# Performance work log

Hardware: AMD Instinct MI355X
Metric: run time of the kernel (lower is better)

## Reference

```python
import jax, jax.numpy as jnp
import numpy as np

B, S_SRC, S_TRG = 128, 512, 128
VIN, VOUT = 128, 128
E, H = 128, 256          # embed, encoder hidden
HD = 2 * H               # decoder hidden = 512 (concat of bi-dir encoder states)
DENC = 2 * H             # encoder output feature dim = 512


def setup_inputs() -> dict:
    key = jax.random.key(0)
    ks = jax.random.split(key, 20)
    g = lambda k, shape: (jax.random.normal(k, shape, jnp.float32) * 0.05)
    inp = {
        "src": jax.random.randint(ks[0], (B, S_SRC), 0, VIN, jnp.int32),
        "trg": jax.random.randint(ks[1], (B, S_TRG), 0, VOUT, jnp.int32),
        # encoder
        "enc_emb": g(ks[2], (VIN, E)),
        "enc_Wih_f": g(ks[3], (4 * H, E)),
        "enc_Whh_f": g(ks[4], (4 * H, H)),
        "enc_b_f": g(ks[5], (4 * H,)),
        "enc_Wih_b": g(ks[6], (4 * H, E)),
        "enc_Whh_b": g(ks[7], (4 * H, H)),
        "enc_b_b": g(ks[8], (4 * H,)),
        # decoder
        "dec_emb": g(ks[9], (VOUT, E)),
        "dec_Wih": g(ks[10], (4 * HD, E + DENC)),
        "dec_Whh": g(ks[11], (4 * HD, HD)),
        "dec_b": g(ks[12], (4 * HD,)),
        # attention: Linear(dec_hid + enc_dim -> HD), v: Linear(HD -> 1)
        "attn_W": g(ks[13], (HD + DENC, HD)),
        "attn_b": g(ks[14], (HD,)),
        "attn_v": g(ks[15], (HD,)),
        # output projection
        "out_W": g(ks[16], (HD, VOUT)),
        "out_b": g(ks[17], (VOUT,)),
    }
    return inp


def _lstm_cell(h, c, x, Wih, Whh, b):
    gates = x @ Wih.T + h @ Whh.T + b               # [B, 4H]
    i, f, gg, o = jnp.split(gates, 4, axis=-1)       # PyTorch gate order i,f,g,o
    i, f, o = jax.nn.sigmoid(i), jax.nn.sigmoid(f), jax.nn.sigmoid(o)
    c = f * c + i * jnp.tanh(gg)
    h = o * jnp.tanh(c)
    return h, c


def _lstm_scan(xs, Wih, Whh, b, reverse=False):
    # xs: [S, B, E] -> hs: [S, B, H] (time-aligned), plus final (h, c)
    Bn, Hn = xs.shape[1], Whh.shape[1]
    init = (jnp.zeros((Bn, Hn), xs.dtype), jnp.zeros((Bn, Hn), xs.dtype))
    def step(carry, x):
        h, c = _lstm_cell(carry[0], carry[1], x, Wih, Whh, b)
        return (h, c), h
    (h, c), hs = jax.lax.scan(step, init, xs, reverse=reverse)
    return hs, h, c


def reference(src, trg, enc_emb, enc_Wih_f, enc_Whh_f, enc_b_f,
              enc_Wih_b, enc_Whh_b, enc_b_b, dec_emb, dec_Wih, dec_Whh,
              dec_b, attn_W, attn_b, attn_v, out_W, out_b):
    # ----- encoder (bidirectional LSTM) -----
    emb = enc_emb[src]                                # [B, S, E]
    xs = jnp.swapaxes(emb, 0, 1)                      # [S, B, E]
    hs_f, hf, cf = _lstm_scan(xs, enc_Wih_f, enc_Whh_f, enc_b_f, reverse=False)
    hs_b, hb, cb = _lstm_scan(xs, enc_Wih_b, enc_Whh_b, enc_b_b, reverse=True)
    enc_out = jnp.swapaxes(jnp.concatenate([hs_f, hs_b], -1), 0, 1)  # [B, S, 2H]
    hidden = jnp.concatenate([hf, hb], -1)            # [B, HD]  (hidden.view(1,B,-1))
    cell = jnp.concatenate([cf, cb], -1)              # [B, HD]

    # attention linear split: energy = tanh([h, enc] @ W + b)
    Wh, We = attn_W[:HD], attn_W[HD:]
    enc_proj = jnp.einsum("bsd,de->bse", enc_out, We)  # [B, S, HD] precomputed

    def dec_step(carry, tok):
        h, c = carry
        e = jnp.tanh(h[:, None, :] @ Wh + enc_proj + attn_b)     # [B, S, HD]
        scores = jnp.einsum("bse,e->bs", e, attn_v)              # [B, S]
        aw = jax.nn.softmax(scores, axis=1)
        ctx = jnp.einsum("bs,bsd->bd", aw, enc_out)              # [B, DENC]
        x = jnp.concatenate([dec_emb[tok], ctx], -1)             # [B, E+DENC]
        h, c = _lstm_cell(h, c, x, dec_Wih, dec_Whh, dec_b)
        logits = h @ out_W + out_b                               # [B, VOUT]
        return (h, c), logits

    # teacher forcing (ratio=1.0): input at step t is trg[:, t-1], t = 1..T-1
    toks = jnp.swapaxes(trg[:, :-1], 0, 1)            # [T-1, B]
    _, logits = jax.lax.scan(dec_step, (hidden, cell), toks)
    logits = jnp.swapaxes(logits, 0, 1)               # [B, T-1, VOUT]
    outputs = jnp.concatenate(
        [jnp.zeros((src.shape[0], 1, VOUT), logits.dtype), logits], axis=1)
    return outputs
```

## Files before the change

kernel.cpp:

```cpp
#include <hip/hip_runtime.h>


typedef _Float16 f16;
typedef _Float16 half8 __attribute__((ext_vector_type(8)));
typedef float f32x4 __attribute__((ext_vector_type(4)));
typedef char char8v __attribute__((ext_vector_type(8)));

#define MFMA16(a, b, c) __builtin_amdgcn_mfma_f32_16x16x32_f16((a), (b), (c), 0, 0, 0)

#define PSCALE (2.5f / 127.f)
#define PINV   (127.f / 2.5f)

__device__ __forceinline__ float fsig(float x) {
    return __builtin_amdgcn_rcpf(1.f + __expf(-x));
}
__device__ __forceinline__ float ftanh(float x) {
    return 1.f - 2.f * __builtin_amdgcn_rcpf(1.f + __expf(2.f * x));
}
__device__ __forceinline__ int frag_idx(int m, int k, int KS) {
    return (((m >> 4) * KS + (k >> 5)) * 64 + (((k >> 3) & 3) * 16 + (m & 15))) * 8 + (k & 7);
}

__global__ __launch_bounds__(256) void k_prep(
    const float* __restrict__ attn_W, const float* __restrict__ out_W,
    const float* __restrict__ enc_emb,
    const float* __restrict__ wihf, const float* __restrict__ wihb,
    const float* __restrict__ whhf, const float* __restrict__ whhb,
    const float* __restrict__ dec_emb, const float* __restrict__ dec_wih,
    const float* __restrict__ dec_whh,
    f16* __restrict__ WhT_sw, f16* __restrict__ outWT_sw,
    f16* __restrict__ whhf_sw, f16* __restrict__ whhb_sw,
    f16* __restrict__ decwih_sw, f16* __restrict__ decwhh_sw,
    f16* __restrict__ WeT, f16* __restrict__ emb16,
    f16* __restrict__ wihf16, f16* __restrict__ wihb16,
    f16* __restrict__ decemb16, float* __restrict__ out)
{
    long i = (long)blockIdx.x * 256 + threadIdx.x;
    if (i >= 3784704L) return;
    long idx = i;
    if (idx < 262144) {
        int j = idx & 7, lane = (idx >> 3) & 63, c = lane & 15, q = lane >> 4;
        int ks = (idx >> 9) & 15, nt = idx >> 13;
        WhT_sw[idx] = (f16)attn_W[(ks * 32 + q * 8 + j) * 512 + nt * 16 + c];
        return;
    }
    idx -= 262144;
    if (idx < 65536) {
        int j = idx & 7, lane = (idx >> 3) & 63, c = lane & 15, q = lane >> 4;
        int ks = (idx >> 9) & 15, nt = idx >> 13;
        outWT_sw[idx] = (f16)out_W[(ks * 32 + q * 8 + j) * 128 + nt * 16 + c];
        return;
    }
    idx -= 65536;
    if (idx < 262144) {
        int j = idx & 7, lane = (idx >> 3) & 63, c = lane & 15, q = lane >> 4;
        int ks = (idx >> 9) & 7, nt = idx >> 12;
        whhf_sw[idx] = (f16)whhf[(nt * 16 + c) * 256 + ks * 32 + q * 8 + j];
        return;
    }
    idx -= 262144;
    if (idx < 262144) {
        int j = idx & 7, lane = (idx >> 3) & 63, c = lane & 15, q = lane >> 4;
        int ks = (idx >> 9) & 7, nt = idx >> 12;
        whhb_sw[idx] = (f16)whhb[(nt * 16 + c) * 256 + ks * 32 + q * 8 + j];
        return;
    }
    idx -= 262144;
    if (idx < 1310720) {
        int j = idx & 7, lane = (idx >> 3) & 63, c = lane & 15, q = lane >> 4;
        int r2 = idx >> 9; int ks = r2 % 20, nt = r2 / 20;
        decwih_sw[idx] = (f16)dec_wih[(nt * 16 + c) * 640 + ks * 32 + q * 8 + j];
        return;
    }
    idx -= 1310720;
    if (idx < 1048576) {
        int j = idx & 7, lane = (idx >> 3) & 63, c = lane & 15, q = lane >> 4;
        int ks = (idx >> 9) & 15, nt = idx >> 13;
        decwhh_sw[idx] = (f16)dec_whh[(nt * 16 + c) * 512 + ks * 32 + q * 8 + j];
        return;
    }
    idx -= 1048576;
    if (idx < 262144) { int e = idx >> 9, d = idx & 511; WeT[idx] = (f16)attn_W[(512 + d) * 512 + e]; return; }
    idx -= 262144;
    if (idx < 16384)  { emb16[idx] = (f16)enc_emb[idx]; return; }
    idx -= 16384;
    if (idx < 131072) { wihf16[idx] = (f16)wihf[idx]; return; }
    idx -= 131072;
    if (idx < 131072) { wihb16[idx] = (f16)wihb[idx]; return; }
    idx -= 131072;
    if (idx < 16384)  { decemb16[idx] = (f16)dec_emb[idx]; return; }
    idx -= 16384;
    if (idx < 16384)  { int b = idx >> 7, v = idx & 127; out[b * 16384 + v] = 0.f; return; }
}

__global__ __launch_bounds__(256) void k_vocab(
    const f16* __restrict__ emb, const f16* __restrict__ wihf,
    const f16* __restrict__ wihb, const float* __restrict__ bf_,
    const float* __restrict__ bb_, f16* __restrict__ xg_vocab)
{
    int bn = blockIdx.x;
    int tid = threadIdx.x, wave = tid >> 6, lane = tid & 63;
    int col = lane & 15, quad = lane >> 4;
    int wr = wave >> 1, wc = wave & 1;

    f32x4 acc[4][4] = {};
    for (int ks = 0; ks < 4; ++ks) {
        int k0 = ks * 32 + quad * 8;
        half8 a[4], bfr[4];
        for (int i = 0; i < 4; ++i)
            a[i] = *(const half8*)(emb + (wr * 64 + i * 16 + col) * 128 + k0);
        for (int j = 0; j < 4; ++j) {
            int n = bn * 128 + wc * 64 + j * 16 + col;
            const f16* wp = (n < 1024) ? (wihf + n * 128) : (wihb + (n - 1024) * 128);
            bfr[j] = *(const half8*)(wp + k0);
        }
        for (int i = 0; i < 4; ++i)
            for (int j = 0; j < 4; ++j)
                acc[i][j] = MFMA16(a[i], bfr[j], acc[i][j]);
    }
    for (int j = 0; j < 4; ++j) {
        int n = bn * 128 + wc * 64 + j * 16 + col;
        float bias = (n < 1024) ? bf_[n] : bb_[n - 1024];
        for (int i = 0; i < 4; ++i) {
            int vbase = wr * 64 + i * 16 + quad * 4;
            for (int r = 0; r < 4; ++r)
                xg_vocab[(vbase + r) * 2048 + n] = (f16)(acc[i][j][r] + bias);
        }
    }
}

__global__ __launch_bounds__(512, 1) void k_enc(
    const int* __restrict__ src, const f16* __restrict__ xg_vocab,
    const f16* __restrict__ whhf_sw, const f16* __restrict__ whhb_sw,
    f16* __restrict__ enc_out, f16* __restrict__ hdec0, float* __restrict__ c_ws)
{
    int blk = blockIdx.x;
    int dir = blk >> 3, bbase = (blk & 7) * 16;
    int tid = threadIdx.x, wave = tid >> 6, lane = tid & 63;
    int col = lane & 15, quad = lane >> 4;
    const f16* whh = dir ? whhb_sw : whhf_sw;

    __shared__ f16 hb[16][264];
    __shared__ f16 xvb[16][1032];
    __shared__ int stall[8192];

    for (int z = tid; z < 16 * 264; z += 512) ((f16*)hb)[z] = (f16)0.f;
    for (int z = tid; z < 8192; z += 512) stall[z] = src[bbase * 512 + z];
    float cc[2][4] = {};

    half8 bst[32];
    #pragma unroll
    for (int g = 0; g < 2; ++g)
        #pragma unroll
        for (int nt = 0; nt < 2; ++nt)
            #pragma unroll
            for (int kk = 0; kk < 8; ++kk) {
                int tile = g * 16 + wave * 2 + nt;
                bst[(g * 2 + nt) * 8 + kk] =
                    *(const half8*)(whh + ((tile * 8 + kk) * 64 + lane) * 8);
            }
    __syncthreads();

    int xrow = tid >> 7, xoff = (tid & 127) * 8;
    half8 xr[4];
    {
        int ts0 = dir ? 511 : 0;
        #pragma unroll
        for (int it = 0; it < 4; ++it) {
            int row = it * 4 + xrow;
            int tok = stall[row * 512 + ts0];
            xr[it] = *(const half8*)(xg_vocab + tok * 2048 + dir * 1024 + xoff);
        }
    }

    int ts_prev = 0;
    for (int t = 0; t < 512; ++t) {
        int ts = dir ? (511 - t) : t;

        if (t > 0) {
            int b = tid >> 5, seg = tid & 31;
            *(half8*)(enc_out + ((size_t)(bbase + b) * 512 + ts_prev) * 512 + dir * 256 + seg * 8) =
                *(const half8*)(&hb[b][seg * 8]);
        }
        #pragma unroll
        for (int it = 0; it < 4; ++it)
            *(half8*)(&xvb[it * 4 + xrow][xoff]) = xr[it];
        half8 a[8];
        #pragma unroll
        for (int kk = 0; kk < 8; ++kk)
            a[kk] = *(const half8*)(&hb[col][kk * 32 + quad * 8]);
        __syncthreads();

        if (t < 511) {
            int tsn = dir ? (510 - t) : (t + 1);
            #pragma unroll
            for (int it = 0; it < 4; ++it) {
                int row = it * 4 + xrow;
                int tok = stall[row * 512 + tsn];
                xr[it] = *(const half8*)(xg_vocab + tok * 2048 + dir * 1024 + xoff);
            }
        }

        f32x4 acc[4][2] = {};
        #pragma unroll
        for (int kk = 0; kk < 8; ++kk) {
            half8 bv[4];
            #pragma unroll
            for (int g = 2; g < 4; ++g)
                #pragma unroll
                for (int nt = 0; nt < 2; ++nt) {
                    int tile = g * 16 + wave * 2 + nt;
                    bv[(g - 2) * 2 + nt] =
                        *(const half8*)(whh + ((tile * 8 + kk) * 64 + lane) * 8);
                }
            #pragma unroll
            for (int g = 0; g < 2; ++g)
                #pragma unroll
                for (int nt = 0; nt < 2; ++nt)
                    acc[g][nt] = MFMA16(a[kk], bst[(g * 2 + nt) * 8 + kk], acc[g][nt]);
            #pragma unroll
            for (int g = 2; g < 4; ++g)
                #pragma unroll
                for (int nt = 0; nt < 2; ++nt)
                    acc[g][nt] = MFMA16(a[kk], bv[(g - 2) * 2 + nt], acc[g][nt]);
        }

        #pragma unroll
        for (int nt = 0; nt < 2; ++nt) {
            int hcol = wave * 32 + nt * 16 + col;
            #pragma unroll
            for (int r = 0; r < 4; ++r) {
                int b = quad * 4 + r;
                float gi = (float)xvb[b][0 * 256 + hcol] + acc[0][nt][r];
                float gf = (float)xvb[b][1 * 256 + hcol] + acc[1][nt][r];
                float gg = (float)xvb[b][2 * 256 + hcol] + acc[2][nt][r];
                float go = (float)xvb[b][3 * 256 + hcol] + acc[3][nt][r];
                float ig = fsig(gi), fg = fsig(gf), g2 = ftanh(gg), og = fsig(go);
                float cv = fg * cc[nt][r] + ig * g2;
                cc[nt][r] = cv;
                float h = og * ftanh(cv);
                hb[b][hcol] = (f16)h;
            }
        }
        __syncthreads();
        ts_prev = ts;
    }

    {
        int b = tid >> 5, seg = tid & 31;
        *(half8*)(enc_out + ((size_t)(bbase + b) * 512 + ts_prev) * 512 + dir * 256 + seg * 8) =
            *(const half8*)(&hb[b][seg * 8]);
    }
    #pragma unroll
    for (int nt = 0; nt < 2; ++nt) {
        int hcol = wave * 32 + nt * 16 + col;
        #pragma unroll
        for (int r = 0; r < 4; ++r) {
            int b = quad * 4 + r;
            int m = bbase + b, k = dir * 256 + hcol;
            hdec0[frag_idx(m, k, 16)] = hb[b][hcol];
            c_ws[m * 512 + k] = cc[nt][r];
        }
    }
}

__global__ __launch_bounds__(256) void k_proj(
    const f16* __restrict__ enc_out, const f16* __restrict__ WeT,
    char* __restrict__ proj8)
{
    int blk = blockIdx.x;
    int bm = blk & 511, bn = blk >> 9;
    int tid = threadIdx.x, wave = tid >> 6, lane = tid & 63;
    int col = lane & 15, quad = lane >> 4;
    int wr = wave >> 1, wc = wave & 1;

    f32x4 acc[4][4] = {};
    for (int ks = 0; ks < 16; ++ks) {
        int k0 = ks * 32 + quad * 8;
        half8 a[4], bfr[4];
        for (int i = 0; i < 4; ++i) {
            int m = bm * 128 + wr * 64 + i * 16 + col;
            a[i] = *(const half8*)(enc_out + (size_t)m * 512 + k0);
        }
        for (int j = 0; j < 4; ++j) {
            int n = bn * 128 + wc * 64 + j * 16 + col;
            bfr[j] = *(const half8*)(WeT + n * 512 + k0);
        }
        for (int i = 0; i < 4; ++i)
            for (int j = 0; j < 4; ++j)
                acc[i][j] = MFMA16(a[i], bfr[j], acc[i][j]);
    }
    for (int j = 0; j < 4; ++j) {
        int n = bn * 128 + wc * 64 + j * 16 + col;
        for (int i = 0; i < 4; ++i) {
            int mbase = bm * 128 + wr * 64 + i * 16 + quad * 4;
            for (int r = 0; r < 4; ++r) {
                float v = acc[i][j][r] * PINV;
                int q = (int)rintf(v);
                q = (q > 127) ? 127 : ((q < -127) ? -127 : q);
                proj8[(size_t)(mbase + r) * 512 + n] = (char)q;
            }
        }
    }
}

__global__ __launch_bounds__(256) void k_qinit(
    const f16* __restrict__ h0_sw, const f16* __restrict__ WhT_sw,
    float* __restrict__ qpart)
{
    int j = blockIdx.x;
    int tid = threadIdx.x, wave = tid >> 6, lane = tid & 63;
    int col = lane & 15, quad = lane >> 4;
    half8 a[2];
    #pragma unroll
    for (int i = 0; i < 2; ++i)
        a[i] = *(const half8*)(h0_sw + (((wave * 2 + i) * 16 + j) * 64 + lane) * 8);
    for (int nt = 0; nt < 32; ++nt) {
        half8 bfr = *(const half8*)(WhT_sw + ((nt * 16 + j) * 64 + lane) * 8);
        f32x4 q0 = {}, q1 = {};
        q0 = MFMA16(a[0], bfr, q0);
        q1 = MFMA16(a[1], bfr, q1);
        #pragma unroll
        for (int r = 0; r < 4; ++r) {
            qpart[(j * 128 + wave * 32 + quad * 4 + r) * 512 + nt * 16 + col] = q0[r];
            qpart[(j * 128 + wave * 32 + 16 + quad * 4 + r) * 512 + nt * 16 + col] = q1[r];
        }
    }
}

__global__ __launch_bounds__(512) void k_att(
    const char* __restrict__ proj8, const f16* __restrict__ enc_out,
    const float* __restrict__ qpart, const float* __restrict__ attn_b,
    const float* __restrict__ attn_v, const int* __restrict__ trg,
    const f16* __restrict__ dec_emb, f16* __restrict__ x_sw,
    float* __restrict__ part_m, float* __restrict__ part_l,
    float* __restrict__ part_ctx, int t)
{
    int blk = blockIdx.x;
    int b = blk >> 1, sh = blk & 1;
    int tid = threadIdx.x, wave = tid >> 6, lane = tid & 63;
    __shared__ float q[512];
    __shared__ float sc[256];
    __shared__ float ctxred[8][512];
    __shared__ float wred[8], wred2[8];

    {
        float s = attn_b[tid];
        #pragma unroll
        for (int jj = 0; jj < 16; ++jj) s += qpart[(jj * 128 + b) * 512 + tid];
        q[tid] = s;
    }
    __syncthreads();

    float qreg[8], vreg[8];
    #pragma unroll
    for (int u = 0; u < 8; ++u) {
        int e = lane * 8 + u;
        qreg[u] = q[e];
        vreg[u] = attn_v[e];
    }
    int sbase = sh * 256;
    for (int ib = 0; ib < 4; ++ib) {
        char8v p[8];
        #pragma unroll
        for (int z = 0; z < 8; ++z) {
            int sl = (ib * 8 + z) * 8 + wave;
            p[z] = *(const char8v*)(proj8 + ((size_t)b * 512 + sbase + sl) * 512 + lane * 8);
        }
        #pragma unroll
        for (int z = 0; z < 8; ++z) {
            int sl = (ib * 8 + z) * 8 + wave;
            float part = 0.f;
            #pragma unroll
            for (int u = 0; u < 8; ++u)
                part += vreg[u] * ftanh(fmaf((float)p[z][u], PSCALE, qreg[u]));
            #pragma unroll
            for (int o = 32; o; o >>= 1) part += __shfl_xor(part, o);
            if (lane == 0) sc[sl] = part;
        }
    }
    __syncthreads();

    float s0 = (tid < 256) ? sc[tid] : -__builtin_inff();
    float mv = s0;
    #pragma unroll
    for (int o = 32; o; o >>= 1) mv = fmaxf(mv, __shfl_xor(mv, o));
    if (lane == 0) wred[wave] = mv;
    __syncthreads();
    float M = wred[0];
    #pragma unroll
    for (int w = 1; w < 8; ++w) M = fmaxf(M, wred[w]);
    float e0 = (tid < 256) ? __expf(s0 - M) : 0.f;
    if (tid < 256) sc[tid] = e0;
    float sm = e0;
    #pragma unroll
    for (int o = 32; o; o >>= 1) sm += __shfl_xor(sm, o);
    if (lane == 0) wred2[wave] = sm;
    __syncthreads();
    float lb = wred2[0];
    #pragma unroll
    for (int w = 1; w < 8; ++w) lb += wred2[w];

    float a8[8] = {};
    for (int ib = 0; ib < 4; ++ib) {
        half8 ev[8];
        float wgt[8];
        #pragma unroll
        for (int z = 0; z < 8; ++z) {
            int sl = (ib * 8 + z) * 8 + wave;
            ev[z] = *(const half8*)(enc_out + ((size_t)b * 512 + sbase + sl) * 512 + lane * 8);
            wgt[z] = sc[sl];
        }
        #pragma unroll
        for (int z = 0; z < 8; ++z)
            #pragma unroll
            for (int u = 0; u < 8; ++u) a8[u] += wgt[z] * (float)ev[z][u];
    }
    #pragma unroll
    for (int u = 0; u < 8; ++u) ctxred[wave][lane * 8 + u] = a8[u];
    __syncthreads();
    float cp = 0.f;
    #pragma unroll
    for (int w = 0; w < 8; ++w) cp += ctxred[w][tid];
    part_ctx[(size_t)blk * 512 + tid] = cp;
    if (tid == 0) { part_m[blk] = M; part_l[blk] = lb; }

    if (sh == 0 && tid < 128) {
        int tok = trg[b * 128 + t];
        x_sw[frag_idx(b, tid, 20)] = dec_emb[tok * 128 + tid];
    }
}

__global__ __launch_bounds__(256) void k_gates(
    f16* __restrict__ x_sw, const f16* __restrict__ hprev_sw,
    const f16* __restrict__ wih_sw, const f16* __restrict__ whh_sw,
    const float* __restrict__ dec_b, float* __restrict__ c_ws,
    f16* __restrict__ hnext_sw, f16* __restrict__ hhist_sw,
    const f16* __restrict__ WhT_sw, float* __restrict__ qpart,
    const float* __restrict__ part_m, const float* __restrict__ part_l,
    const float* __restrict__ part_ctx, int t)
{
    int jb = blockIdx.x;
    int j = jb >> 1, mh = jb & 1;
    int tid = threadIdx.x, wave = tid >> 6, lane = tid & 63;
    int col = lane & 15, quad = lane >> 4;
    __shared__ f16 hsl[64][40];
    __shared__ float gm[64][2];

    if (tid < 64) {
        int bb = mh * 64 + tid;
        float m0 = part_m[bb * 2 + 0], m1 = part_m[bb * 2 + 1];
        float l0 = part_l[bb * 2 + 0], l1 = part_l[bb * 2 + 1];
        float M = fmaxf(m0, m1);
        float g0 = __expf(m0 - M), g1 = __expf(m1 - M);
        float inv = 1.f / (g0 * l0 + g1 * l1);
        gm[tid][0] = g0 * inv;
        gm[tid][1] = g1 * inv;
    }
    __syncthreads();
    for (int z = tid; z < 32768; z += 256) {
        int lr = z >> 9, d = z & 511;
        int bb = mh * 64 + lr;
        float c = gm[lr][0] * part_ctx[(size_t)(bb * 2 + 0) * 512 + d]
                + gm[lr][1] * part_ctx[(size_t)(bb * 2 + 1) * 512 + d];
        x_sw[frag_idx(bb, 128 + d, 20)] = (f16)c;
    }
    __syncthreads();

    f32x4 acc[8] = {};
    for (int ks = 0; ks < 36; ++ks) {
        int mtile = mh * 4 + wave;
        half8 a = (ks < 20)
            ? *(const half8*)(x_sw + ((mtile * 20 + ks) * 64 + lane) * 8)
            : *(const half8*)(hprev_sw + ((mtile * 16 + (ks - 20)) * 64 + lane) * 8);
        half8 bv[8];
        #pragma unroll
        for (int jt = 0; jt < 8; ++jt) {
            int g = jt >> 1, u2 = jt & 1;
            int ntile = g * 32 + j * 2 + u2;
            bv[jt] = (ks < 20)
                ? *(const half8*)(wih_sw + ((ntile * 20 + ks) * 64 + lane) * 8)
                : *(const half8*)(whh_sw + ((ntile * 16 + (ks - 20)) * 64 + lane) * 8);
        }
        #pragma unroll
        for (int jt = 0; jt < 8; ++jt)
            acc[jt] = MFMA16(a, bv[jt], acc[jt]);
    }
    float bias[8];
    #pragma unroll
    for (int jt = 0; jt < 8; ++jt) {
        int g = jt >> 1, u2 = jt & 1;
        bias[jt] = dec_b[g * 512 + j * 32 + u2 * 16 + col];
    }
    #pragma unroll
    for (int r = 0; r < 4; ++r) {
        int lb = wave * 16 + quad * 4 + r;
        int bb = mh * 64 + lb;
        #pragma unroll
        for (int u2 = 0; u2 < 2; ++u2) {
            int hl = u2 * 16 + col, hcol = j * 32 + hl;
            float gi = acc[0 + u2][r] + bias[0 + u2];
            float gf = acc[2 + u2][r] + bias[2 + u2];
            float gg = acc[4 + u2][r] + bias[4 + u2];
            float go = acc[6 + u2][r] + bias[6 + u2];
            float ig = fsig(gi), fg = fsig(gf), g2 = ftanh(gg), og = fsig(go);
            float cv = fg * c_ws[bb * 512 + hcol] + ig * g2;
            c_ws[bb * 512 + hcol] = cv;
            float h = og * ftanh(cv);
            f16 h16 = (f16)h;
            int fidx = frag_idx(bb, hcol, 16);
            hnext_sw[fidx] = h16;
            hhist_sw[t * 65536 + fidx] = h16;
            hsl[lb][hl] = h16;
        }
    }
    half8 aq = *(const half8*)(&hsl[wave * 16 + col][quad * 8]);
    for (int nt = 0; nt < 32; ++nt) {
        half8 bq = *(const half8*)(WhT_sw + ((nt * 16 + j) * 64 + lane) * 8);
        f32x4 q0 = {};
        q0 = MFMA16(aq, bq, q0);
        #pragma unroll
        for (int r = 0; r < 4; ++r)
            qpart[(j * 128 + mh * 64 + wave * 16 + quad * 4 + r) * 512 + nt * 16 + col] = q0[r];
    }
}

__global__ __launch_bounds__(256) void k_logits(
    const f16* __restrict__ hhist_sw, const f16* __restrict__ outWT_sw,
    const float* __restrict__ out_b, float* __restrict__ out)
{
    int bt = blockIdx.x;
    int tid = threadIdx.x, wave = tid >> 6, lane = tid & 63;
    int col = lane & 15, quad = lane >> 4;
    f32x4 acc[2][8] = {};
    for (int ks = 0; ks < 16; ++ks) {
        half8 a[2];
        #pragma unroll
        for (int i = 0; i < 2; ++i)
            a[i] = *(const half8*)(hhist_sw + bt * 65536 + (((wave * 2 + i) * 16 + ks) * 64 + lane) * 8);
        half8 bv[8];
        #pragma unroll
        for (int jt = 0; jt < 8; ++jt)
            bv[jt] = *(const half8*)(outWT_sw + ((jt * 16 + ks) * 64 + lane) * 8);
        #pragma unroll
        for (int jt = 0; jt < 8; ++jt) {
            acc[0][jt] = MFMA16(a[0], bv[jt], acc[0][jt]);
            acc[1][jt] = MFMA16(a[1], bv[jt], acc[1][jt]);
        }
    }
    #pragma unroll
    for (int jt = 0; jt < 8; ++jt) {
        float bias = out_b[jt * 16 + col];
        #pragma unroll
        for (int i = 0; i < 2; ++i)
            #pragma unroll
            for (int r = 0; r < 4; ++r) {
                int br = wave * 32 + i * 16 + quad * 4 + r;
                out[br * 16384 + (bt + 1) * 128 + jt * 16 + col] = acc[i][jt][r] + bias;
            }
    }
}

extern "C" void kernel_launch(void* const* d_in, const int* in_sizes, int n_in,
                              void* d_out, int out_size, void* d_ws, size_t ws_size,
                              hipStream_t stream)
{
    (void)in_sizes; (void)n_in; (void)out_size;
    if (ws_size < 130000000) return;

    const int*   src     = (const int*)d_in[0];
    const int*   trg     = (const int*)d_in[1];
    const float* enc_emb = (const float*)d_in[2];
    const float* wihf    = (const float*)d_in[3];
    const float* whhf    = (const float*)d_in[4];
    const float* bf_     = (const float*)d_in[5];
    const float* wihb    = (const float*)d_in[6];
    const float* whhb    = (const float*)d_in[7];
    const float* bb_     = (const float*)d_in[8];
    const float* dec_emb = (const float*)d_in[9];
    const float* dec_wih = (const float*)d_in[10];
    const float* dec_whh = (const float*)d_in[11];
    const float* dec_b   = (const float*)d_in[12];
    const float* attn_W  = (const float*)d_in[13];
    const float* attn_b  = (const float*)d_in[14];
    const float* attn_v  = (const float*)d_in[15];
    const float* out_W   = (const float*)d_in[16];
    const float* out_b   = (const float*)d_in[17];
    float* out = (float*)d_out;

    char* p = (char*)d_ws;
    auto carve = [&](size_t n) { char* r = p; p += ((n + 255) & ~(size_t)255); return r; };
    f16*   enc_out   = (f16*)  carve(67108864);
    char*  proj8     = (char*) carve(33554432);
    f16*   WhT_sw    = (f16*)  carve(524288);
    f16*   WeT       = (f16*)  carve(524288);
    f16*   outWT_sw  = (f16*)  carve(131072);
    f16*   emb16     = (f16*)  carve(32768);
    f16*   wihf16    = (f16*)  carve(262144);
    f16*   wihb16    = (f16*)  carve(262144);
    f16*   whhf_sw   = (f16*)  carve(524288);
    f16*   whhb_sw   = (f16*)  carve(524288);
    f16*   decemb16  = (f16*)  carve(32768);
    f16*   decwih_sw = (f16*)  carve(2621440);
    f16*   decwhh_sw = (f16*)  carve(2097152);
    float* qpart     = (float*)carve(4194304);
    f16*   hdec0     = (f16*)  carve(131072);
    f16*   hdec1     = (f16*)  carve(131072);
    float* c_ws      = (float*)carve(262144);
    f16*   x_sw      = (f16*)  carve(163840);
    f16*   hhist_sw  = (f16*)  carve(16646144);
    f16*   xg_vocab  = (f16*)  carve(524288);
    float* part_m    = (float*)carve(2048);
    float* part_l    = (float*)carve(2048);
    float* part_ctx  = (float*)carve(524288);

    k_prep<<<14784, 256, 0, stream>>>(attn_W, out_W, enc_emb, wihf, wihb, whhf, whhb,
                                      dec_emb, dec_wih, dec_whh,
                                      WhT_sw, outWT_sw, whhf_sw, whhb_sw,
                                      decwih_sw, decwhh_sw, WeT, emb16,
                                      wihf16, wihb16, decemb16, out);
    k_vocab<<<16, 256, 0, stream>>>(emb16, wihf16, wihb16, bf_, bb_, xg_vocab);
    k_enc<<<16, 512, 0, stream>>>(src, xg_vocab, whhf_sw, whhb_sw, enc_out, hdec0, c_ws);
    k_proj<<<2048, 256, 0, stream>>>(enc_out, WeT, proj8);
    k_qinit<<<16, 256, 0, stream>>>(hdec0, WhT_sw, qpart);
    for (int t = 0; t < 127; ++t) {
        k_att<<<256, 512, 0, stream>>>(proj8, enc_out, qpart, attn_b, attn_v,
                                       trg, decemb16, x_sw, part_m, part_l,
                                       part_ctx, t);
        f16* hin  = (t & 1) ? hdec1 : hdec0;
        f16* hout = (t & 1) ? hdec0 : hdec1;
        k_gates<<<32, 256, 0, stream>>>(x_sw, hin, decwih_sw, decwhh_sw, dec_b,
                                        c_ws, hout, hhist_sw, WhT_sw, qpart,
                                        part_m, part_l, part_ctx, t);
    }
    k_logits<<<127, 256, 0, stream>>>(hhist_sw, outWT_sw, out_b, out);
}
```

Baseline: 13.39 ms.

## Fuse decoder timestep loop into one persistent kernel with grid barriers

Replaces the 254 per-step launches of the attention and gate kernels with a single persistent kernel of 256 blocks that loops over all 127 decoder steps. Blocks synchronise through atomic-counter grid barriers in global memory, and the gate work runs on 16 of the blocks, each now covering all 128 batch rows. The aim is to remove kernel launch overhead and inter-kernel gaps on this latency-bound recurrence. In exchange, 240 blocks sit idle during the gate phase, the gate work loses half its previous parallelism, and correctness depends on all 256 blocks being resident at once.

```diff
diff --git a/kernel.cpp b/kernel.cpp
--- a/kernel.cpp
+++ b/kernel.cpp
@@ -19,6 +19,23 @@
 }
 __device__ __forceinline__ int frag_idx(int m, int k, int KS) {
     return (((m >> 4) * KS + (k >> 5)) * 64 + (((k >> 3) & 3) * 16 + (m & 15))) * 8 + (k & 7);
+}
+
+__device__ __forceinline__ void gbar(unsigned* ctr, bool arriver, unsigned target) {
+    __syncthreads();
+    if (threadIdx.x == 0) {
+        if (arriver)
+            __hip_atomic_fetch_add(ctr, 1u, __ATOMIC_RELEASE, __HIP_MEMORY_SCOPE_AGENT);
+        while (__hip_atomic_load(ctr, __ATOMIC_RELAXED, __HIP_MEMORY_SCOPE_AGENT) < target)
+            __builtin_amdgcn_s_sleep(8);
+        (void)__hip_atomic_load(ctr, __ATOMIC_ACQUIRE, __HIP_MEMORY_SCOPE_AGENT);
+    }
+    __syncthreads();
+}
+
+__global__ void k_zero(unsigned* __restrict__ s)
+{
+    if (threadIdx.x < 64) s[threadIdx.x] = 0u;
 }
 
 __global__ __launch_bounds__(256) void k_prep(
@@ -328,200 +345,200 @@
     }
 }
 
-__global__ __launch_bounds__(512) void k_att(
+__global__ __launch_bounds__(512, 2) void k_decode(
     const char* __restrict__ proj8, const f16* __restrict__ enc_out,
-    const float* __restrict__ qpart, const float* __restrict__ attn_b,
-    const float* __restrict__ attn_v, const int* __restrict__ trg,
+    float* __restrict__ qpart, const float* __restrict__ attn_bp,
+    const float* __restrict__ attn_vp, const int* __restrict__ trg,
     const f16* __restrict__ dec_emb, f16* __restrict__ x_sw,
     float* __restrict__ part_m, float* __restrict__ part_l,
-    float* __restrict__ part_ctx, int t)
+    float* __restrict__ part_ctx, f16* __restrict__ hdec0,
+    f16* __restrict__ hdec1, const f16* __restrict__ wih_sw,
+    const f16* __restrict__ whh_sw, const float* __restrict__ dec_bp,
+    float* __restrict__ c_ws, f16* __restrict__ hhist_sw,
+    const f16* __restrict__ WhT_sw, unsigned* __restrict__ syncv)
 {
     int blk = blockIdx.x;
+    int tid = threadIdx.x, wave = tid >> 6, lane = tid & 63;
+    int col = lane & 15, quad = lane >> 4;
     int b = blk >> 1, sh = blk & 1;
-    int tid = threadIdx.x, wave = tid >> 6, lane = tid & 63;
+    int sbase = sh * 256;
+
     __shared__ float q[512];
     __shared__ float sc[256];
     __shared__ float ctxred[8][512];
     __shared__ float wred[8], wred2[8];
-
-    {
-        float s = attn_b[tid];
-        #pragma unroll
-        for (int jj = 0; jj < 16; ++jj) s += qpart[(jj * 128 + b) * 512 + tid];
-        q[tid] = s;
-    }
-    __syncthreads();
-
-    float qreg[8], vreg[8];
+    __shared__ f16 hsl[128][40];
+    __shared__ float gm[128][2];
+
+    float vreg[8];
     #pragma unroll
-    for (int u = 0; u < 8; ++u) {
-        int e = lane * 8 + u;
-        qreg[u] = q[e];
-        vreg[u] = attn_v[e];
-    }
-    int sbase = sh * 256;
-    for (int ib = 0; ib < 4; ++ib) {
-        char8v p[8];
-        #pragma unroll
-        for (int z = 0; z < 8; ++z) {
-            int sl = (ib * 8 + z) * 8 + wave;
-            p[z] = *(const char8v*)(proj8 + ((size_t)b * 512 + sbase + sl) * 512 + lane * 8);
-        }
-        #pragma unroll
-        for (int z = 0; z < 8; ++z) {
-            int sl = (ib * 8 + z) * 8 + wave;
-            float part = 0.f;
-            #pragma unroll
-            for (int u = 0; u < 8; ++u)
-                part += vreg[u] * ftanh(fmaf((float)p[z][u], PSCALE, qreg[u]));
-            #pragma unroll
-            for (int o = 32; o; o >>= 1) part += __shfl_xor(part, o);
-            if (lane == 0) sc[sl] = part;
-        }
-    }
-    __syncthreads();
-
-    float s0 = (tid < 256) ? sc[tid] : -__builtin_inff();
-    float mv = s0;
-    #pragma unroll
-    for (int o = 32; o; o >>= 1) mv = fmaxf(mv, __shfl_xor(mv, o));
-    if (lane == 0) wred[wave] = mv;
-    __syncthreads();
-    float M = wred[0];
-    #pragma unroll
-    for (int w = 1; w < 8; ++w) M = fmaxf(M, wred[w]);
-    float e0 = (tid < 256) ? __expf(s0 - M) : 0.f;
-    if (tid < 256) sc[tid] = e0;
-    float sm = e0;
-    #pragma unroll
-    for (int o = 32; o; o >>= 1) sm += __shfl_xor(sm, o);
-    if (lane == 0) wred2[wave] = sm;
-    __syncthreads();
-    float lb = wred2[0];
-    #pragma unroll
-    for (int w = 1; w < 8; ++w) lb += wred2[w];
-
-    float a8[8] = {};
-    for (int ib = 0; ib < 4; ++ib) {
-        half8 ev[8];
-        float wgt[8];
-        #pragma unroll
-        for (int z = 0; z < 8; ++z) {
-            int sl = (ib * 8 + z) * 8 + wave;
-            ev[z] = *(const half8*)(enc_out + ((size_t)b * 512 + sbase + sl) * 512 + lane * 8);
-            wgt[z] = sc[sl];
-        }
-        #pragma unroll
-        for (int z = 0; z < 8; ++z)
-            #pragma unroll
-            for (int u = 0; u < 8; ++u) a8[u] += wgt[z] * (float)ev[z][u];
-    }
-    #pragma unroll
-    for (int u = 0; u < 8; ++u) ctxred[wave][lane * 8 + u] = a8[u];
-    __syncthreads();
-    float cp = 0.f;
-    #pragma unroll
-    for (int w = 0; w < 8; ++w) cp += ctxred[w][tid];
-    part_ctx[(size_t)blk * 512 + tid] = cp;
-    if (tid == 0) { part_m[blk] = M; part_l[blk] = lb; }
-
-    if (sh == 0 && tid < 128) {
-        int tok = trg[b * 128 + t];
-        x_sw[frag_idx(b, tid, 20)] = dec_emb[tok * 128 + tid];
-    }
-}
-
-__global__ __launch_bounds__(256) void k_gates(
-    f16* __restrict__ x_sw, const f16* __restrict__ hprev_sw,
-    const f16* __restrict__ wih_sw, const f16* __restrict__ whh_sw,
-    const float* __restrict__ dec_b, float* __restrict__ c_ws,
-    f16* __restrict__ hnext_sw, f16* __restrict__ hhist_sw,
-    const f16* __restrict__ WhT_sw, float* __restrict__ qpart,
-    const float* __restrict__ part_m, const float* __restrict__ part_l,
-    const float* __restrict__ part_ctx, int t)
-{
-    int jb = blockIdx.x;
-    int j = jb >> 1, mh = jb & 1;
-    int tid = threadIdx.x, wave = tid >> 6, lane = tid & 63;
-    int col = lane & 15, quad = lane >> 4;
-    __shared__ f16 hsl[64][40];
-    __shared__ float gm[64][2];
-
-    if (tid < 64) {
-        int bb = mh * 64 + tid;
-        float m0 = part_m[bb * 2 + 0], m1 = part_m[bb * 2 + 1];
-        float l0 = part_l[bb * 2 + 0], l1 = part_l[bb * 2 + 1];
-        float M = fmaxf(m0, m1);
-        float g0 = __expf(m0 - M), g1 = __expf(m1 - M);
-        float inv = 1.f / (g0 * l0 + g1 * l1);
-        gm[tid][0] = g0 * inv;
-        gm[tid][1] = g1 * inv;
-    }
-    __syncthreads();
-    for (int z = tid; z < 32768; z += 256) {
-        int lr = z >> 9, d = z & 511;
-        int bb = mh * 64 + lr;
-        float c = gm[lr][0] * part_ctx[(size_t)(bb * 2 + 0) * 512 + d]
-                + gm[lr][1] * part_ctx[(size_t)(bb * 2 + 1) * 512 + d];
-        x_sw[frag_idx(bb, 128 + d, 20)] = (f16)c;
-    }
-    __syncthreads();
-
-    f32x4 acc[8] = {};
-    for (int ks = 0; ks < 36; ++ks) {
-        int mtile = mh * 4 + wave;
-        half8 a = (ks < 20)
-            ? *(const half8*)(x_sw + ((mtile * 20 + ks) * 64 + lane) * 8)
-            : *(const half8*)(hprev_sw + ((mtile * 16 + (ks - 20)) * 64 + lane) * 8);
-        half8 bv[8];
-        #pragma unroll
-        for (int jt = 0; jt < 8; ++jt) {
-            int g = jt >> 1, u2 = jt & 1;
-            int ntile = g * 32 + j * 2 + u2;
-            bv[jt] = (ks < 20)
-                ? *(const half8*)(wih_sw + ((ntile * 20 + ks) * 64 + lane) * 8)
-                : *(const half8*)(whh_sw + ((ntile * 16 + (ks - 20)) * 64 + lane) * 8);
-        }
-        #pragma unroll
-        for (int jt = 0; jt < 8; ++jt)
-            acc[jt] = MFMA16(a, bv[jt], acc[jt]);
-    }
-    float bias[8];
-    #pragma unroll
-    for (int jt = 0; jt < 8; ++jt) {
-        int g = jt >> 1, u2 = jt & 1;
-        bias[jt] = dec_b[g * 512 + j * 32 + u2 * 16 + col];
-    }
-    #pragma unroll
-    for (int r = 0; r < 4; ++r) {
-        int lb = wave * 16 + quad * 4 + r;
-        int bb = mh * 64 + lb;
-        #pragma unroll
-        for (int u2 = 0; u2 < 2; ++u2) {
-            int hl = u2 * 16 + col, hcol = j * 32 + hl;
-            float gi = acc[0 + u2][r] + bias[0 + u2];
-            float gf = acc[2 + u2][r] + bias[2 + u2];
-            float gg = acc[4 + u2][r] + bias[4 + u2];
-            float go = acc[6 + u2][r] + bias[6 + u2];
-            float ig = fsig(gi), fg = fsig(gf), g2 = ftanh(gg), og = fsig(go);
-            float cv = fg * c_ws[bb * 512 + hcol] + ig * g2;
-            c_ws[bb * 512 + hcol] = cv;
-            float h = og * ftanh(cv);
-            f16 h16 = (f16)h;
-            int fidx = frag_idx(bb, hcol, 16);
-            hnext_sw[fidx] = h16;
-            hhist_sw[t * 65536 + fidx] = h16;
-            hsl[lb][hl] = h16;
-        }
-    }
-    half8 aq = *(const half8*)(&hsl[wave * 16 + col][quad * 8]);
-    for (int nt = 0; nt < 32; ++nt) {
-        half8 bq = *(const half8*)(WhT_sw + ((nt * 16 + j) * 64 + lane) * 8);
-        f32x4 q0 = {};
-        q0 = MFMA16(aq, bq, q0);
-        #pragma unroll
-        for (int r = 0; r < 4; ++r)
-            qpart[(j * 128 + mh * 64 + wave * 16 + quad * 4 + r) * 512 + nt * 16 + col] = q0[r];
+    for (int u = 0; u < 8; ++u) vreg[u] = attn_vp[lane * 8 + u];
+    float ab = attn_bp[tid];
+
+    for (int t = 0; t < 127; ++t) {
+        {
+            float s = ab;
+            #pragma unroll
+            for (int jj = 0; jj < 16; ++jj) s += qpart[(jj * 128 + b) * 512 + tid];
+            q[tid] = s;
+        }
+        __syncthreads();
+        float qreg[8];
+        #pragma unroll
+        for (int u = 0; u < 8; ++u) qreg[u] = q[lane * 8 + u];
+
+        for (int ib = 0; ib < 4; ++ib) {
+            char8v p[8];
+            #pragma unroll
+            for (int z = 0; z < 8; ++z) {
+                int sl = (ib * 8 + z) * 8 + wave;
+                p[z] = *(const char8v*)(proj8 + ((size_t)b * 512 + sbase + sl) * 512 + lane * 8);
+            }
+            #pragma unroll
+            for (int z = 0; z < 8; ++z) {
+                int sl = (ib * 8 + z) * 8 + wave;
+                float part = 0.f;
+                #pragma unroll
+                for (int u = 0; u < 8; ++u)
+                    part += vreg[u] * ftanh(fmaf((float)p[z][u], PSCALE, qreg[u]));
+                #pragma unroll
+                for (int o = 32; o; o >>= 1) part += __shfl_xor(part, o);
+                if (lane == 0) sc[sl] = part;
+            }
+        }
+        __syncthreads();
+
+        float s0 = (tid < 256) ? sc[tid] : -__builtin_inff();
+        float mv = s0;
+        #pragma unroll
+        for (int o = 32; o; o >>= 1) mv = fmaxf(mv, __shfl_xor(mv, o));
+        if (lane == 0) wred[wave] = mv;
+        __syncthreads();
+        float M = wred[0];
+        #pragma unroll
+        for (int w = 1; w < 8; ++w) M = fmaxf(M, wred[w]);
+        float e0 = (tid < 256) ? __expf(s0 - M) : 0.f;
+        if (tid < 256) sc[tid] = e0;
+        float sm = e0;
+        #pragma unroll
+        for (int o = 32; o; o >>= 1) sm += __shfl_xor(sm, o);
+        if (lane == 0) wred2[wave] = sm;
+        __syncthreads();
+        float lsum = wred2[0];
+        #pragma unroll
+        for (int w = 1; w < 8; ++w) lsum += wred2[w];
+
+        float a8[8] = {};
+        for (int ib = 0; ib < 4; ++ib) {
+            half8 ev[8];
+            float wgt[8];
+            #pragma unroll
+            for (int z = 0; z < 8; ++z) {
+                int sl = (ib * 8 + z) * 8 + wave;
+                ev[z] = *(const half8*)(enc_out + ((size_t)b * 512 + sbase + sl) * 512 + lane * 8);
+                wgt[z] = sc[sl];
+            }
+            #pragma unroll
+            for (int z = 0; z < 8; ++z)
+                #pragma unroll
+                for (int u = 0; u < 8; ++u) a8[u] += wgt[z] * (float)ev[z][u];
+        }
+        #pragma unroll
+        for (int u = 0; u < 8; ++u) ctxred[wave][lane * 8 + u] = a8[u];
+        __syncthreads();
+        float cp = 0.f;
+        #pragma unroll
+        for (int w = 0; w < 8; ++w) cp += ctxred[w][tid];
+        part_ctx[(size_t)blk * 512 + tid] = cp;
+        if (tid == 0) { part_m[blk] = M; part_l[blk] = lsum; }
+
+        if (sh == 0 && tid < 128) {
+            int tok = trg[b * 128 + t];
+            x_sw[frag_idx(b, tid, 20)] = dec_emb[tok * 128 + tid];
+        }
+
+        gbar(&syncv[0], true, 256u * (unsigned)(t + 1));
+
+        if (blk < 16) {
+            int j = blk;
+            if (tid < 128) {
+                float m0 = part_m[tid * 2 + 0], m1 = part_m[tid * 2 + 1];
+                float l0 = part_l[tid * 2 + 0], l1 = part_l[tid * 2 + 1];
+                float Mx = fmaxf(m0, m1);
+                float g0 = __expf(m0 - Mx), g1 = __expf(m1 - Mx);
+                float inv = 1.f / (g0 * l0 + g1 * l1);
+                gm[tid][0] = g0 * inv;
+                gm[tid][1] = g1 * inv;
+            }
+            __syncthreads();
+            for (int z = tid; z < 65536; z += 512) {
+                int lr = z >> 9, d = z & 511;
+                float cval = gm[lr][0] * part_ctx[(size_t)(lr * 2 + 0) * 512 + d]
+                           + gm[lr][1] * part_ctx[(size_t)(lr * 2 + 1) * 512 + d];
+                x_sw[frag_idx(lr, 128 + d, 20)] = (f16)cval;
+            }
+            __syncthreads();
+
+            const f16* hprev = (t & 1) ? hdec1 : hdec0;
+            f16* hnext = (t & 1) ? hdec0 : hdec1;
+
+            f32x4 acc[8] = {};
+            for (int ks = 0; ks < 36; ++ks) {
+                half8 a = (ks < 20)
+                    ? *(const half8*)(x_sw + ((wave * 20 + ks) * 64 + lane) * 8)
+                    : *(const half8*)(hprev + ((wave * 16 + (ks - 20)) * 64 + lane) * 8);
+                half8 bv[8];
+                #pragma unroll
+                for (int jt = 0; jt < 8; ++jt) {
+                    int g = jt >> 1, u2 = jt & 1;
+                    int ntile = g * 32 + j * 2 + u2;
+                    bv[jt] = (ks < 20)
+                        ? *(const half8*)(wih_sw + ((ntile * 20 + ks) * 64 + lane) * 8)
+                        : *(const half8*)(whh_sw + ((ntile * 16 + (ks - 20)) * 64 + lane) * 8);
+                }
+                #pragma unroll
+                for (int jt = 0; jt < 8; ++jt)
+                    acc[jt] = MFMA16(a, bv[jt], acc[jt]);
+            }
+            float bias[8];
+            #pragma unroll
+            for (int jt = 0; jt < 8; ++jt) {
+                int g = jt >> 1, u2 = jt & 1;
+                bias[jt] = dec_bp[g * 512 + j * 32 + u2 * 16 + col];
+            }
+            #pragma unroll
+            for (int r = 0; r < 4; ++r) {
+                int bb = wave * 16 + quad * 4 + r;
+                #pragma unroll
+                for (int u2 = 0; u2 < 2; ++u2) {
+                    int hl = u2 * 16 + col, hcol = j * 32 + hl;
+                    float gi = acc[0 + u2][r] + bias[0 + u2];
+                    float gf = acc[2 + u2][r] + bias[2 + u2];
+                    float gg = acc[4 + u2][r] + bias[4 + u2];
+                    float go = acc[6 + u2][r] + bias[6 + u2];
+                    float ig = fsig(gi), fg = fsig(gf), g2 = ftanh(gg), og = fsig(go);
+                    float cv = fg * c_ws[bb * 512 + hcol] + ig * g2;
+                    c_ws[bb * 512 + hcol] = cv;
+                    float h = og * ftanh(cv);
+                    f16 h16 = (f16)h;
+                    int fidx = frag_idx(bb, hcol, 16);
+                    hnext[fidx] = h16;
+                    hhist_sw[t * 65536 + fidx] = h16;
+                    hsl[bb][hl] = h16;
+                }
+            }
+            half8 aq = *(const half8*)(&hsl[wave * 16 + col][quad * 8]);
+            for (int nt = 0; nt < 32; ++nt) {
+                half8 bq = *(const half8*)(WhT_sw + ((nt * 16 + j) * 64 + lane) * 8);
+                f32x4 q0 = {};
+                q0 = MFMA16(aq, bq, q0);
+                #pragma unroll
+                for (int r = 0; r < 4; ++r)
+                    qpart[(j * 128 + wave * 16 + quad * 4 + r) * 512 + nt * 16 + col] = q0[r];
+            }
+        }
+
+        gbar(&syncv[1], blk < 16, 16u * (unsigned)(t + 1));
     }
 }
 
@@ -613,7 +630,9 @@
     float* part_m    = (float*)carve(2048);
     float* part_l    = (float*)carve(2048);
     float* part_ctx  = (float*)carve(524288);
-
+    unsigned* syncv  = (unsigned*)carve(256);
+
+    k_zero<<<1, 64, 0, stream>>>(syncv);
     k_prep<<<14784, 256, 0, stream>>>(attn_W, out_W, enc_emb, wihf, wihb, whhf, whhb,
                                       dec_emb, dec_wih, dec_whh,
                                       WhT_sw, outWT_sw, whhf_sw, whhb_sw,
@@ -623,15 +642,12 @@
     k_enc<<<16, 512, 0, stream>>>(src, xg_vocab, whhf_sw, whhb_sw, enc_out, hdec0, c_ws);
     k_proj<<<2048, 256, 0, stream>>>(enc_out, WeT, proj8);
     k_qinit<<<16, 256, 0, stream>>>(hdec0, WhT_sw, qpart);
-    for (int t = 0; t < 127; ++t) {
-        k_att<<<256, 512, 0, stream>>>(proj8, enc_out, qpart, attn_b, attn_v,
-                                       trg, decemb16, x_sw, part_m, part_l,
-                                       part_ctx, t);
-        f16* hin  = (t & 1) ? hdec1 : hdec0;
-        f16* hout = (t & 1) ? hdec0 : hdec1;
-        k_gates<<<32, 256, 0, stream>>>(x_sw, hin, decwih_sw, decwhh_sw, dec_b,
-                                        c_ws, hout, hhist_sw, WhT_sw, qpart,
-                                        part_m, part_l, part_ctx, t);
-    }
+
+    k_decode<<<256, 512, 0, stream>>>(proj8, enc_out, qpart, attn_b, attn_v,
+                                      trg, decemb16, x_sw, part_m, part_l,
+                                      part_ctx, hdec0, hdec1, decwih_sw,
+                                      decwhh_sw, dec_b, c_ws, hhist_sw,
+                                      WhT_sw, syncv);
+
     k_logits<<<127, 256, 0, stream>>>(hhist_sw, outWT_sw, out_b, out);
 }
```

Measured after the change: 21.50 ms. 60.6% more time.

## Fuse attention and gate kernels per step with in-kernel flag sync

Applied to the files above, without the earlier changes.

Merges the per-step attention and LSTM-gate launches into one kernel. 32 blocks finish the previous step's gates while 256 attention blocks spin-wait on per-block flags released by an atomic counter, and a final standalone gate launch handles the last step. This halves the number of launches in the decoder loop and lets attention blocks start as soon as their inputs are ready instead of waiting at a kernel boundary. The cost is spin-wait overhead, and the scheme relies on the gate blocks being scheduled alongside the waiting attention blocks to avoid deadlock.

```diff
diff --git a/kernel.cpp b/kernel.cpp
--- a/kernel.cpp
+++ b/kernel.cpp
@@ -19,6 +19,11 @@
 }
 __device__ __forceinline__ int frag_idx(int m, int k, int KS) {
     return (((m >> 4) * KS + (k >> 5)) * 64 + (((k >> 3) & 3) * 16 + (m & 15))) * 8 + (k & 7);
+}
+
+__global__ void k_zero(unsigned* __restrict__ s)
+{
+    for (int z = threadIdx.x; z < 4112; z += 256) s[z] = 0u;
 }
 
 __global__ __launch_bounds__(256) void k_prep(
@@ -328,38 +333,162 @@
     }
 }
 
-__global__ __launch_bounds__(512) void k_att(
+__global__ __launch_bounds__(512, 4) void k_step(
     const char* __restrict__ proj8, const f16* __restrict__ enc_out,
-    const float* __restrict__ qpart, const float* __restrict__ attn_b,
-    const float* __restrict__ attn_v, const int* __restrict__ trg,
+    float* __restrict__ qpart, const float* __restrict__ attn_bp,
+    const float* __restrict__ attn_vp, const int* __restrict__ trg,
     const f16* __restrict__ dec_emb, f16* __restrict__ x_sw,
     float* __restrict__ part_m, float* __restrict__ part_l,
-    float* __restrict__ part_ctx, int t)
+    float* __restrict__ part_ctx, f16* __restrict__ hdec0,
+    f16* __restrict__ hdec1, const f16* __restrict__ wih_sw,
+    const f16* __restrict__ whh_sw, const float* __restrict__ dec_bp,
+    float* __restrict__ c_ws, f16* __restrict__ hhist_sw,
+    const f16* __restrict__ WhT_sw, unsigned* __restrict__ flags, int tt)
 {
     int blk = blockIdx.x;
-    int b = blk >> 1, sh = blk & 1;
     int tid = threadIdx.x, wave = tid >> 6, lane = tid & 63;
+    int col = lane & 15, quad = lane >> 4;
+
     __shared__ float q[512];
     __shared__ float sc[256];
     __shared__ float ctxred[8][512];
     __shared__ float wred[8], wred2[8];
+    __shared__ f16 hsl[64][40];
+    __shared__ float gm[64][2];
+    __shared__ int islast;
+
+    if (blk < 32) {
+        int tg = tt - 1;
+        if (tg >= 0) {
+            int j = blk >> 1, mh = blk & 1;
+            if (tid < 64) {
+                int bb = mh * 64 + tid;
+                float m0 = part_m[bb * 2 + 0], m1 = part_m[bb * 2 + 1];
+                float l0 = part_l[bb * 2 + 0], l1 = part_l[bb * 2 + 1];
+                float M = fmaxf(m0, m1);
+                float g0 = __expf(m0 - M), g1 = __expf(m1 - M);
+                float inv = 1.f / (g0 * l0 + g1 * l1);
+                gm[tid][0] = g0 * inv;
+                gm[tid][1] = g1 * inv;
+            }
+            __syncthreads();
+            for (int z = tid; z < 32768; z += 512) {
+                int lr = z >> 9, d = z & 511;
+                int bb = mh * 64 + lr;
+                float c = gm[lr][0] * part_ctx[(size_t)(bb * 2 + 0) * 512 + d]
+                        + gm[lr][1] * part_ctx[(size_t)(bb * 2 + 1) * 512 + d];
+                x_sw[frag_idx(bb, 128 + d, 20)] = (f16)c;
+            }
+            __syncthreads();
+
+            if (tid < 256) {
+                const f16* hprev = (tg & 1) ? hdec1 : hdec0;
+                f16* hnext = (tg & 1) ? hdec0 : hdec1;
+
+                f32x4 acc[8] = {};
+                for (int ks = 0; ks < 36; ++ks) {
+                    int mtile = mh * 4 + wave;
+                    half8 a = (ks < 20)
+                        ? *(const half8*)(x_sw + ((mtile * 20 + ks) * 64 + lane) * 8)
+                        : *(const half8*)(hprev + ((mtile * 16 + (ks - 20)) * 64 + lane) * 8);
+                    half8 bv[8];
+                    #pragma unroll
+                    for (int jt = 0; jt < 8; ++jt) {
+                        int g = jt >> 1, u2 = jt & 1;
+                        int ntile = g * 32 + j * 2 + u2;
+                        bv[jt] = (ks < 20)
+                            ? *(const half8*)(wih_sw + ((ntile * 20 + ks) * 64 + lane) * 8)
+                            : *(const half8*)(whh_sw + ((ntile * 16 + (ks - 20)) * 64 + lane) * 8);
+                    }
+                    #pragma unroll
+                    for (int jt = 0; jt < 8; ++jt)
+                        acc[jt] = MFMA16(a, bv[jt], acc[jt]);
+                }
+                float bias[8];
+                #pragma unroll
+                for (int jt = 0; jt < 8; ++jt) {
+                    int g = jt >> 1, u2 = jt & 1;
+                    bias[jt] = dec_bp[g * 512 + j * 32 + u2 * 16 + col];
+                }
+                #pragma unroll
+                for (int r = 0; r < 4; ++r) {
+                    int lb = wave * 16 + quad * 4 + r;
+                    int bb = mh * 64 + lb;
+                    #pragma unroll
+                    for (int u2 = 0; u2 < 2; ++u2) {
+                        int hl = u2 * 16 + col, hcol = j * 32 + hl;
+                        float gi = acc[0 + u2][r] + bias[0 + u2];
+                        float gf = acc[2 + u2][r] + bias[2 + u2];
+                        float gg = acc[4 + u2][r] + bias[4 + u2];
+                        float go = acc[6 + u2][r] + bias[6 + u2];
+                        float ig = fsig(gi), fg = fsig(gf), g2 = ftanh(gg), og = fsig(go);
+                        float cv = fg * c_ws[bb * 512 + hcol] + ig * g2;
+                        c_ws[bb * 512 + hcol] = cv;
+                        float h = og * ftanh(cv);
+                        f16 h16 = (f16)h;
+                        int fidx = frag_idx(bb, hcol, 16);
+                        hnext[fidx] = h16;
+                        hhist_sw[tg * 65536 + fidx] = h16;
+                        hsl[lb][hl] = h16;
+                    }
+                }
+                half8 aq = *(const half8*)(&hsl[wave * 16 + col][quad * 8]);
+                for (int nt = 0; nt < 32; ++nt) {
+                    half8 bq = *(const half8*)(WhT_sw + ((nt * 16 + j) * 64 + lane) * 8);
+                    f32x4 q0 = {};
+                    q0 = MFMA16(aq, bq, q0);
+                    #pragma unroll
+                    for (int r = 0; r < 4; ++r)
+                        qpart[(j * 128 + mh * 64 + wave * 16 + quad * 4 + r) * 512 + nt * 16 + col] = q0[r];
+                }
+            }
+
+            __syncthreads();
+            if (tid == 0) {
+                unsigned old = __hip_atomic_fetch_add(flags, 1u, __ATOMIC_ACQ_REL,
+                                                      __HIP_MEMORY_SCOPE_AGENT);
+                islast = (old == (unsigned)(32 * tt - 1)) ? 1 : 0;
+            }
+            __syncthreads();
+            if (islast && tid < 256)
+                __hip_atomic_store(flags + 16 + tid * 16, (unsigned)tt,
+                                   __ATOMIC_RELEASE, __HIP_MEMORY_SCOPE_AGENT);
+        }
+        return;
+    }
+
+    int ab = blk - 32;
+    int b = ab >> 1, sh = ab & 1;
+    int sbase = sh * 256;
+
+    float vreg[8];
+    #pragma unroll
+    for (int u = 0; u < 8; ++u) vreg[u] = attn_vp[lane * 8 + u];
+    float abias = attn_bp[tid];
+
+    if (tt > 0) {
+        if (tid == 0) {
+            while (__hip_atomic_load(flags + 16 + ab * 16, __ATOMIC_RELAXED,
+                                     __HIP_MEMORY_SCOPE_AGENT) < (unsigned)tt)
+                __builtin_amdgcn_s_sleep(16);
+            (void)__hip_atomic_load(flags + 16 + ab * 16, __ATOMIC_ACQUIRE,
+                                    __HIP_MEMORY_SCOPE_AGENT);
+        }
+        __syncthreads();
+    }
 
     {
-        float s = attn_b[tid];
+        float s = abias;
         #pragma unroll
         for (int jj = 0; jj < 16; ++jj) s += qpart[(jj * 128 + b) * 512 + tid];
         q[tid] = s;
     }
     __syncthreads();
 
-    float qreg[8], vreg[8];
-    #pragma unroll
-    for (int u = 0; u < 8; ++u) {
-        int e = lane * 8 + u;
-        qreg[u] = q[e];
-        vreg[u] = attn_v[e];
-    }
-    int sbase = sh * 256;
+    float qreg[8];
+    #pragma unroll
+    for (int u = 0; u < 8; ++u) qreg[u] = q[lane * 8 + u];
+
     for (int ib = 0; ib < 4; ++ib) {
         char8v p[8];
         #pragma unroll
@@ -397,9 +526,9 @@
     for (int o = 32; o; o >>= 1) sm += __shfl_xor(sm, o);
     if (lane == 0) wred2[wave] = sm;
     __syncthreads();
-    float lb = wred2[0];
-    #pragma unroll
-    for (int w = 1; w < 8; ++w) lb += wred2[w];
+    float lsum = wred2[0];
+    #pragma unroll
+    for (int w = 1; w < 8; ++w) lsum += wred2[w];
 
     float a8[8] = {};
     for (int ib = 0; ib < 4; ++ib) {
@@ -422,11 +551,11 @@
     float cp = 0.f;
     #pragma unroll
     for (int w = 0; w < 8; ++w) cp += ctxred[w][tid];
-    part_ctx[(size_t)blk * 512 + tid] = cp;
-    if (tid == 0) { part_m[blk] = M; part_l[blk] = lb; }
+    part_ctx[(size_t)ab * 512 + tid] = cp;
+    if (tid == 0) { part_m[ab] = M; part_l[ab] = lsum; }
 
     if (sh == 0 && tid < 128) {
-        int tok = trg[b * 128 + t];
+        int tok = trg[b * 128 + tt];
         x_sw[frag_idx(b, tid, 20)] = dec_emb[tok * 128 + tid];
     }
 }
@@ -613,7 +742,9 @@
     float* part_m    = (float*)carve(2048);
     float* part_l    = (float*)carve(2048);
     float* part_ctx  = (float*)carve(524288);
-
+    unsigned* flagsv = (unsigned*)carve(16448);
+
+    k_zero<<<1, 256, 0, stream>>>(flagsv);
     k_prep<<<14784, 256, 0, stream>>>(attn_W, out_W, enc_emb, wihf, wihb, whhf, whhb,
                                       dec_emb, dec_wih, dec_whh,
                                       WhT_sw, outWT_sw, whhf_sw, whhb_sw,
@@ -623,15 +754,16 @@
     k_enc<<<16, 512, 0, stream>>>(src, xg_vocab, whhf_sw, whhb_sw, enc_out, hdec0, c_ws);
     k_proj<<<2048, 256, 0, stream>>>(enc_out, WeT, proj8);
     k_qinit<<<16, 256, 0, stream>>>(hdec0, WhT_sw, qpart);
-    for (int t = 0; t < 127; ++t) {
-        k_att<<<256, 512, 0, stream>>>(proj8, enc_out, qpart, attn_b, attn_v,
-                                       trg, decemb16, x_sw, part_m, part_l,
-                                       part_ctx, t);
-        f16* hin  = (t & 1) ? hdec1 : hdec0;
-        f16* hout = (t & 1) ? hdec0 : hdec1;
-        k_gates<<<32, 256, 0, stream>>>(x_sw, hin, decwih_sw, decwhh_sw, dec_b,
-                                        c_ws, hout, hhist_sw, WhT_sw, qpart,
-                                        part_m, part_l, part_ctx, t);
-    }
+
+    for (int tt = 0; tt < 127; ++tt)
+        k_step<<<288, 512, 0, stream>>>(proj8, enc_out, qpart, attn_b, attn_v,
+                                        trg, decemb16, x_sw, part_m, part_l,
+                                        part_ctx, hdec0, hdec1, decwih_sw,
+                                        decwhh_sw, dec_b, c_ws, hhist_sw,
+                                        WhT_sw, flagsv, tt);
+    k_gates<<<32, 256, 0, stream>>>(x_sw, hdec0, decwih_sw, decwhh_sw, dec_b,
+                                    c_ws, hdec1, hhist_sw, WhT_sw, qpart,
+                                    part_m, part_l, part_ctx, 126);
+
     k_logits<<<127, 256, 0, stream>>>(hhist_sw, outWT_sw, out_b, out);
 }
```

After: 12.81 ms. 1.05x faster.
